# Performance work log

Hardware: AMD Instinct MI355X
Metric: run time of the kernel (lower is better)

Reference implementation:

```python
import jax, jax.numpy as jnp
import numpy as np

jax.config.update("jax_enable_x64", True)

# Module hyperparameters (from init_kwargs)
NUM_EMB = 1_000_000
EMB_DIM = 128
COMPRESSION = 1.0 / 64.0
WEIGHT_SIZE = int(NUM_EMB * EMB_DIM * COMPRESSION)  # 2_000_000 (1D compressed table)

# Hash constants matching the CUDA kernel's multiplicative hash:
# hashed_idx = (index * P1 + dim * P2) mod weight_size
P1 = np.uint64(9824516537)
P2 = np.uint64(57857966300227)

BATCH = 16384
BAG_LEN = 50


def _hashed_idx(indices):
    # indices: [N] int -> hashed positions [N, EMB_DIM] into the 1D weight table
    flat = indices.reshape(-1).astype(jnp.uint64)
    dims = jnp.arange(EMB_DIM, dtype=jnp.uint64)
    h = (flat[:, None] * P1 + dims[None, :] * P2) % jnp.uint64(WEIGHT_SIZE)
    return h.astype(jnp.int64)


def setup_inputs() -> dict:
    key = jax.random.key(0)
    k1, k2 = jax.random.split(key)
    indices = jax.random.randint(k1, (BATCH, BAG_LEN), 0, NUM_EMB, dtype=jnp.int64)
    # reset_parameters(): init.normal_(weight)
    weight = jax.random.normal(k2, (WEIGHT_SIZE,), dtype=jnp.float32)
    return {"weight": weight, "indices": indices}


def reference(weight, indices):
    # 2D indices path: each row is one bag of fixed length; mode='sum'.
    B, L = indices.shape
    hidx = _hashed_idx(indices)                      # [B*L, D]
    emb = weight[hidx].reshape(B, L, EMB_DIM)        # gather from compressed table
    return emb.sum(axis=1)                           # [B, D] per-bag sum
```

## Files before the change

kernel.cpp:

```cpp
#include <hip/hip_runtime.h>
#include <stdint.h>


#define WS       2000000
#define EMB_DIM  128
#define BAG_LEN  50
#define BATCH    16384

#define NBLK     256
#define NTHR     1024
#define BAGS_PB  64
#define NPAIR    32
#define SPT      4
#define EXTP     208
#define THALF    32768
#define NREGD    62
#define SBIG     300227u
#define SENT     0x10000000u

#define OFF_T1   65536
#define OFF_EXT  131072
#define SMEM_SZ  157696

#define GLOAD_LDS16(gp, lp)                                            \
    __builtin_amdgcn_global_load_lds(                                  \
        (const __attribute__((address_space(1))) uint32_t*)(gp),       \
        (__attribute__((address_space(3))) uint32_t*)(lp), 16, 0, 0)

__global__ __launch_bounds__(1024) void conv_bf16(
    const float* __restrict__ w, uint16_t* __restrict__ o)
{
    const int i = (blockIdx.x * 1024 + threadIdx.x) * 4;
    if (i >= WS) return;
    const float4 f = *(const float4*)(w + i);
    uint32_t u0 = __float_as_uint(f.x), u1 = __float_as_uint(f.y);
    uint32_t u2 = __float_as_uint(f.z), u3 = __float_as_uint(f.w);
    ushort4 r;
    r.x = (uint16_t)((u0 + 0x7FFFu + ((u0 >> 16) & 1u)) >> 16);
    r.y = (uint16_t)((u1 + 0x7FFFu + ((u1 >> 16) & 1u)) >> 16);
    r.z = (uint16_t)((u2 + 0x7FFFu + ((u2 >> 16) & 1u)) >> 16);
    r.w = (uint16_t)((u3 + 0x7FFFu + ((u3 >> 16) & 1u)) >> 16);
    *(ushort4*)(o + i) = r;
}

__global__ __launch_bounds__(NTHR, 4) void heb_bf16(
    const uint16_t* __restrict__ wbf,
    const int*      __restrict__ indices,
    float*          __restrict__ out)
{
    __shared__ __align__(16) uint8_t smem[SMEM_SZ];

    const int tid     = threadIdx.x;
    const int d       = tid & 127;
    const int g       = tid >> 7;
    const int bagBase = blockIdx.x * BAGS_PB;

    uint16_t* tile0 = (uint16_t*)&smem[0];
    uint32_t* ext   = (uint32_t*)&smem[OFF_EXT];
    uint32_t* araw  = (uint32_t*)&smem[OFF_T1];
    uint32_t* S     = (uint32_t*)&smem[OFF_T1 + 13312];

    for (int s = tid; s < (THALF >> 3); s += NTHR)
        GLOAD_LDS16(wbf + (s << 3), tile0 + (s << 3));

    for (int p = tid; p < NPAIR * EXTP; p += NTHR) ext[p] = SENT;
    for (int p = tid; p < BAGS_PB * BAG_LEN; p += NTHR) {
        uint32_t b = (uint32_t)p / 50u;
        uint32_t i = (uint32_t)p - b * 50u;
        uint64_t idx = (uint64_t)(uint32_t)indices[bagBase * BAG_LEN + p];
        araw[b * 52 + i] = (uint32_t)((idx * 9824516537ull) % (uint64_t)WS);
    }
    __syncthreads();

    for (int p = tid; p < BAGS_PB * BAG_LEN; p += NTHR) {
        uint32_t b = (uint32_t)p / 50u;
        uint32_t i = (uint32_t)p - b * 50u;
        uint32_t v = araw[b * 52 + i];
        int rank = 0;
        for (int q = 0; q < BAG_LEN; ++q) {
            uint32_t w = araw[b * 52 + q];
            rank += (w < v || (w == v && q < (int)i)) ? 1 : 0;
        }
        S[b * 52 + rank] = v;
    }
    __syncthreads();

    for (int p = tid; p < BAGS_PB * BAG_LEN; p += NTHR) {
        uint32_t bag = (uint32_t)p / 50u;
        uint32_t i   = (uint32_t)p - bag * 50u;
        uint32_t pr  = bag >> 1, b = bag & 1u;
        uint32_t v = S[bag * 52 + i];
        const uint32_t* T = &S[(bag ^ 1u) * 52];
        uint32_t key = b ? v + 1u : v;
        int lo = 0, hi = 50;
        while (lo < hi) {
            int mid = (lo + hi) >> 1;
            bool lt = T[mid] < key;
            lo = lt ? mid + 1 : lo;
            hi = lt ? hi : mid;
        }
        uint32_t* eo = ext + pr * EXTP;
        int rk = (int)i + lo;
        eo[rk]       = (v << 1) | b;
        eo[rk + 100] = ((v + (uint32_t)WS) << 1) | b;
    }
    __syncthreads();

    const uint32_t c  = ((uint32_t)d * SBIG) % (uint32_t)WS;
    const uint32_t C2 = (uint32_t)(((int)c - WS) * 2);
    const uint32_t limit2 = ((uint32_t)WS - c) << 1;

    const char* kp4[SPT];
    uint32_t    K4[SPT];
    float       s0r[SPT], s1r[SPT];
#pragma unroll
    for (int qi = 0; qi < SPT; ++qi) {
        const uint32_t* eo = ext + ((g << 2) + qi) * EXTP;
        int lo = 0, hi = 100;
        while (lo < hi) {
            int mid = (lo + hi) >> 1;
            bool lt = eo[mid] < limit2;
            lo = lt ? mid + 1 : lo;
            hi = lt ? hi : mid;
        }
        kp4[qi] = (const char*)(eo + lo);
        K4[qi]  = eo[lo];
        s0r[qi] = 0.0f; s1r[qi] = 0.0f;
    }
    __syncthreads();

    for (int r = 0; r < NREGD; ++r) {
        if (r + 1 < NREGD) {
            const int lo2  = (r + 1) * THALF;
            const int len2 = (THALF < WS - lo2) ? THALF : (WS - lo2);
            uint16_t* dst = (uint16_t*)&smem[((r + 1) & 1) ? OFF_T1 : 0];
            for (int s = tid; s < (len2 >> 3); s += NTHR)
                GLOAD_LDS16(wbf + lo2 + (s << 3), dst + (s << 3));
        }

        const int rlo = r * THALF;
        const int len = (THALF < WS - rlo) ? THALF : (WS - rlo);
        const uint32_t TB  = (r & 1) ? (uint32_t)OFF_T1 : 0u;
        const uint32_t CLr = C2 + TB - ((uint32_t)rlo << 1);
        const uint32_t LIM = ((uint32_t)len << 1) + TB;

#pragma unroll
        for (int qi = 0; qi < SPT; ++qi) {
            const char* kp = kp4[qi];
            uint32_t K_ = K4[qi];
            float s0 = s0r[qi], s1 = s1r[qi];
            uint32_t u = K_ + CLr;
            while (u < LIM) {
                const uint32_t raw =
                    *(const uint16_t*)(smem + (u & ~1u));
                kp += 4;
                const uint32_t Kn = *(const uint32_t*)kp;
                const float v = __uint_as_float(raw << 16);
                const bool odd = (u & 1u) != 0u;
                s0 += odd ? 0.0f : v;
                s1 += odd ? v : 0.0f;
                K_ = Kn;
                u  = Kn + CLr;
            }
            kp4[qi] = kp; K4[qi] = K_;
            s0r[qi] = s0; s1r[qi] = s1;
        }
        __syncthreads();
    }

#pragma unroll
    for (int qi = 0; qi < SPT; ++qi) {
        const int bag = (g << 3) + (qi << 1);
        out[(size_t)(bagBase + bag) * EMB_DIM + d]     = s0r[qi];
        out[(size_t)(bagBase + bag + 1) * EMB_DIM + d] = s1r[qi];
    }
}

#define RSIZE_FB 32768
#define NREG_FB  62
#define EXT_N    104
#define SENT4    0x10000000u

__global__ __launch_bounds__(NTHR, 4) void heb_single(
    const float* __restrict__ weight,
    const int*   __restrict__ indices,
    float*       __restrict__ out)
{
    __shared__ __align__(16) float tile[RSIZE_FB];
    __shared__ uint32_t ext4[BAGS_PB][EXT_N];
    const int tid = threadIdx.x, d = tid & 127, bag_lo = tid >> 7;
    const int bagBase = blockIdx.x * BAGS_PB;
    uint32_t* araw = (uint32_t*)&tile[0];
    for (int p = tid; p < BAGS_PB * BAG_LEN; p += NTHR) {
        uint32_t g = (uint32_t)p / 50u, i = (uint32_t)p - g * 50u;
        uint64_t idx = (uint64_t)(uint32_t)indices[bagBase * BAG_LEN + p];
        araw[g * 52 + i] = (uint32_t)((idx * 9824516537ull) % (uint64_t)WS);
    }
    __syncthreads();
    for (int p = tid; p < BAGS_PB * BAG_LEN; p += NTHR) {
        uint32_t g = (uint32_t)p / 50u, i = (uint32_t)p - g * 50u;
        uint32_t v = araw[g * 52 + i];
        int rank = 0;
        for (int q = 0; q < BAG_LEN; ++q) {
            uint32_t w = araw[g * 52 + q];
            rank += (w < v || (w == v && q < (int)i)) ? 1 : 0;
        }
        ext4[g][rank] = v << 2;
        ext4[g][rank + 50] = (v + (uint32_t)WS) << 2;
    }
    for (int p = tid; p < BAGS_PB * 4; p += NTHR)
        ext4[p >> 2][100 + (p & 3)] = SENT4;
    __syncthreads();
    const uint32_t c = ((uint32_t)d * SBIG) % (uint32_t)WS;
    const uint32_t C4 = (uint32_t)(((int)c - WS) * 4);
    const uint32_t wmc4 = ((uint32_t)WS - c) << 2;
    uint32_t t4[8], h4[8]; float sm[8];
#pragma unroll
    for (int k = 0; k < 8; ++k) {
        const uint32_t* eg = &ext4[(bag_lo << 3) + k][0];
        int nlow = 0;
        for (int q = 0; q < BAG_LEN; ++q) nlow += (eg[q] < wmc4) ? 1 : 0;
        t4[k] = (uint32_t)nlow << 2; h4[k] = eg[nlow] + C4; sm[k] = 0.0f;
    }
    for (int r = 0; r < NREG_FB; ++r) {
        const int lo = r * RSIZE_FB;
        const int len = (RSIZE_FB < WS - lo) ? RSIZE_FB : (WS - lo);
        __syncthreads();
        for (int s = tid; s < (len >> 2); s += NTHR)
            GLOAD_LDS16(weight + lo + (s << 2), &tile[s << 2]);
        __syncthreads();
        const uint32_t lo4 = ((uint32_t)lo) << 2;
        const uint32_t hi4 = (r == NREG_FB - 1) ? (uint32_t)(4 * WS)
                                                : lo4 + ((uint32_t)RSIZE_FB << 2);
        const char* tb = (const char*)&tile[0];
#pragma unroll
        for (int k = 0; k < 8; ++k) {
            const char* eg = (const char*)&ext4[(bag_lo << 3) + k][0];
            uint32_t t_ = t4[k], h_ = h4[k]; float s_ = sm[k];
            while (h_ < hi4) {
                s_ += *(const float*)(tb + (h_ - lo4));
                t_ += 4u;
                h_ = *(const uint32_t*)(eg + t_) + C4;
            }
            t4[k] = t_; h4[k] = h_; sm[k] = s_;
        }
    }
#pragma unroll
    for (int k = 0; k < 8; ++k)
        out[(size_t)(bagBase + (bag_lo << 3) + k) * EMB_DIM + d] = sm[k];
}

extern "C" void kernel_launch(void* const* d_in, const int* in_sizes, int n_in,
                              void* d_out, int out_size, void* d_ws, size_t ws_size,
                              hipStream_t stream)
{
    const float* weight  = (const float*)d_in[0];
    const int*   indices = (const int*)d_in[1];
    float*       out     = (float*)d_out;

    if (ws_size >= (size_t)WS * sizeof(uint16_t)) {
        uint16_t* wbf = (uint16_t*)d_ws;
        conv_bf16<<<(WS / 4 + 1023) / 1024, 1024, 0, stream>>>(weight, wbf);
        heb_bf16<<<NBLK, NTHR, 0, stream>>>(wbf, indices, out);
    } else {
        heb_single<<<NBLK, NTHR, 0, stream>>>(weight, indices, out);
    }
}
```

Before: 230.0 us.

## Split block work: sweep 48 bags through LDS, gather 16 bags directly from global

Each block now sends only 48 of its 64 bags through the region-sweeping LDS scheme, which walks the whole bf16 table in 62 regions. The other two thread groups gather the remaining 16 bags straight from the global bf16 table, one bag element per region iteration, which overlaps random global loads with the LDS sweep. The intent is to spread the sweep's work over fewer bags and to use the otherwise idle memory bandwidth for direct gathers. In exchange it adds load imbalance between the two kinds of thread groups and uncoalesced global accesses, and the extension-list pointer is now an index.

```diff
diff --git a/kernel.cpp b/kernel.cpp
--- a/kernel.cpp
+++ b/kernel.cpp
@@ -10,7 +10,9 @@
 #define NBLK     256
 #define NTHR     1024
 #define BAGS_PB  64
-#define NPAIR    32
+#define SWBAGS   48
+#define GBAGS    16
+#define NPAIR    24
 #define SPT      4
 #define EXTP     208
 #define THALF    32768
@@ -20,7 +22,8 @@
 
 #define OFF_T1   65536
 #define OFF_EXT  131072
-#define SMEM_SZ  157696
+#define OFF_AG   151040
+#define SMEM_SZ  154240
 
 #define GLOAD_LDS16(gp, lp)                                            \
     __builtin_amdgcn_global_load_lds(                                  \
@@ -57,8 +60,9 @@
 
     uint16_t* tile0 = (uint16_t*)&smem[0];
     uint32_t* ext   = (uint32_t*)&smem[OFF_EXT];
+    uint32_t* ag    = (uint32_t*)&smem[OFF_AG];
     uint32_t* araw  = (uint32_t*)&smem[OFF_T1];
-    uint32_t* S     = (uint32_t*)&smem[OFF_T1 + 13312];
+    uint32_t* S     = (uint32_t*)&smem[OFF_T1 + 9984];
 
     for (int s = tid; s < (THALF >> 3); s += NTHR)
         GLOAD_LDS16(wbf + (s << 3), tile0 + (s << 3));
@@ -68,11 +72,13 @@
         uint32_t b = (uint32_t)p / 50u;
         uint32_t i = (uint32_t)p - b * 50u;
         uint64_t idx = (uint64_t)(uint32_t)indices[bagBase * BAG_LEN + p];
-        araw[b * 52 + i] = (uint32_t)((idx * 9824516537ull) % (uint64_t)WS);
-    }
-    __syncthreads();
-
-    for (int p = tid; p < BAGS_PB * BAG_LEN; p += NTHR) {
+        uint32_t a = (uint32_t)((idx * 9824516537ull) % (uint64_t)WS);
+        if (b < SWBAGS) araw[b * 52 + i] = a;
+        else            ag[(b - SWBAGS) * 50 + i] = a;
+    }
+    __syncthreads();
+
+    for (int p = tid; p < SWBAGS * BAG_LEN; p += NTHR) {
         uint32_t b = (uint32_t)p / 50u;
         uint32_t i = (uint32_t)p - b * 50u;
         uint32_t v = araw[b * 52 + i];
@@ -85,7 +91,7 @@
     }
     __syncthreads();
 
-    for (int p = tid; p < BAGS_PB * BAG_LEN; p += NTHR) {
+    for (int p = tid; p < SWBAGS * BAG_LEN; p += NTHR) {
         uint32_t bag = (uint32_t)p / 50u;
         uint32_t i   = (uint32_t)p - bag * 50u;
         uint32_t pr  = bag >> 1, b = bag & 1u;
@@ -110,22 +116,36 @@
     const uint32_t C2 = (uint32_t)(((int)c - WS) * 2);
     const uint32_t limit2 = ((uint32_t)WS - c) << 1;
 
-    const char* kp4[SPT];
-    uint32_t    K4[SPT];
-    float       s0r[SPT], s1r[SPT];
-#pragma unroll
-    for (int qi = 0; qi < SPT; ++qi) {
-        const uint32_t* eo = ext + ((g << 2) + qi) * EXTP;
-        int lo = 0, hi = 100;
-        while (lo < hi) {
-            int mid = (lo + hi) >> 1;
-            bool lt = eo[mid] < limit2;
-            lo = lt ? mid + 1 : lo;
-            hi = lt ? hi : mid;
-        }
-        kp4[qi] = (const char*)(eo + lo);
-        K4[qi]  = eo[lo];
-        s0r[qi] = 0.0f; s1r[qi] = 0.0f;
+    uint32_t kq4[SPT] = {0, 0, 0, 0}, K4[SPT] = {0, 0, 0, 0};
+    float    s0r[SPT] = {0, 0, 0, 0}, s1r[SPT] = {0, 0, 0, 0};
+    uint32_t gck[8];
+    float    gacc[8];
+    int      bagG = 0, agB = 0, d0 = 0;
+
+    if (g < 6) {
+#pragma unroll
+        for (int qi = 0; qi < SPT; ++qi) {
+            const uint32_t rbase = (uint32_t)((g << 2) + qi) * EXTP;
+            int lo = 0, hi = 100;
+            while (lo < hi) {
+                int mid = (lo + hi) >> 1;
+                bool lt = ext[rbase + (uint32_t)mid] < limit2;
+                lo = lt ? mid + 1 : lo;
+                hi = lt ? hi : mid;
+            }
+            kq4[qi] = rbase + (uint32_t)lo;
+            K4[qi]  = ext[rbase + (uint32_t)lo];
+        }
+    } else {
+        const int L = tid & 127;
+        bagG = (g << 3) + (L >> 4);
+        d0   = L & 15;
+        agB  = (bagG - SWBAGS) * 50;
+#pragma unroll
+        for (int k = 0; k < 8; ++k) {
+            gck[k]  = ((uint32_t)(d0 + 16 * k) * SBIG) % (uint32_t)WS;
+            gacc[k] = 0.0f;
+        }
     }
     __syncthreads();
 
@@ -138,41 +158,57 @@
                 GLOAD_LDS16(wbf + lo2 + (s << 3), dst + (s << 3));
         }
 
-        const int rlo = r * THALF;
-        const int len = (THALF < WS - rlo) ? THALF : (WS - rlo);
-        const uint32_t TB  = (r & 1) ? (uint32_t)OFF_T1 : 0u;
-        const uint32_t CLr = C2 + TB - ((uint32_t)rlo << 1);
-        const uint32_t LIM = ((uint32_t)len << 1) + TB;
-
+        if (g < 6) {
+            const int rlo = r * THALF;
+            const int len = (THALF < WS - rlo) ? THALF : (WS - rlo);
+            const uint32_t TB  = (r & 1) ? (uint32_t)OFF_T1 : 0u;
+            const uint32_t CLr = C2 + TB - ((uint32_t)rlo << 1);
+            const uint32_t LIM = ((uint32_t)len << 1) + TB;
+
+#pragma unroll
+            for (int qi = 0; qi < SPT; ++qi) {
+                uint32_t kq = kq4[qi], K = K4[qi];
+                float s0 = s0r[qi], s1 = s1r[qi];
+                uint32_t u = K + CLr;
+                while (u < LIM) {
+                    const uint32_t raw =
+                        *(const uint16_t*)(smem + (u & ~1u));
+                    K = ext[kq + 1u];
+                    ++kq;
+                    const float v = __uint_as_float(raw << 16);
+                    const bool odd = (u & 1u) != 0u;
+                    s0 += odd ? 0.0f : v;
+                    s1 += odd ? v : 0.0f;
+                    u = K + CLr;
+                }
+                kq4[qi] = kq; K4[qi] = K;
+                s0r[qi] = s0; s1r[qi] = s1;
+            }
+        } else if (r < BAG_LEN) {
+            const uint32_t a = ag[agB + r];
+#pragma unroll
+            for (int k = 0; k < 8; ++k) {
+                uint32_t u = a + gck[k];
+                u = (u >= (uint32_t)WS) ? u - (uint32_t)WS : u;
+                const uint32_t raw = (uint32_t)wbf[u];
+                gacc[k] += __uint_as_float(raw << 16);
+            }
+        }
+        __syncthreads();
+    }
+
+    if (g < 6) {
 #pragma unroll
         for (int qi = 0; qi < SPT; ++qi) {
-            const char* kp = kp4[qi];
-            uint32_t K_ = K4[qi];
-            float s0 = s0r[qi], s1 = s1r[qi];
-            uint32_t u = K_ + CLr;
-            while (u < LIM) {
-                const uint32_t raw =
-                    *(const uint16_t*)(smem + (u & ~1u));
-                kp += 4;
-                const uint32_t Kn = *(const uint32_t*)kp;
-                const float v = __uint_as_float(raw << 16);
-                const bool odd = (u & 1u) != 0u;
-                s0 += odd ? 0.0f : v;
-                s1 += odd ? v : 0.0f;
-                K_ = Kn;
-                u  = Kn + CLr;
-            }
-            kp4[qi] = kp; K4[qi] = K_;
-            s0r[qi] = s0; s1r[qi] = s1;
-        }
-        __syncthreads();
-    }
-
-#pragma unroll
-    for (int qi = 0; qi < SPT; ++qi) {
-        const int bag = (g << 3) + (qi << 1);
-        out[(size_t)(bagBase + bag) * EMB_DIM + d]     = s0r[qi];
-        out[(size_t)(bagBase + bag + 1) * EMB_DIM + d] = s1r[qi];
+            const int bag = (g << 3) + (qi << 1);
+            out[(size_t)(bagBase + bag) * EMB_DIM + d]     = s0r[qi];
+            out[(size_t)(bagBase + bag + 1) * EMB_DIM + d] = s1r[qi];
+        }
+    } else {
+#pragma unroll
+        for (int k = 0; k < 8; ++k)
+            out[(size_t)(bagBase + bagG) * EMB_DIM + (d0 + 16 * k)] =
+                gacc[k];
     }
 }
 
```

After: 236.6 us. 2.8% more time.

## Split bags between LDS-streaming blocks and direct-gather blocks, shrink tile for occupancy

Applied to the files above, without the earlier changes.

The bag work is split in two. 48 of each 64-bag group stay on the LDS-streaming path, and the other 16 bags go to 256 extra blocks that gather bf16 weights straight from global memory. The streaming path drops double buffering and uses one smaller single tile, so LDS use falls enough to allow 8 blocks per CU. In exchange it adds two barriers per region and more regions. The aim is to overlap the random-gather blocks with the streaming blocks and raise occupancy, at the cost of serialising the tile load with compute.

```diff
diff --git a/kernel.cpp b/kernel.cpp
--- a/kernel.cpp
+++ b/kernel.cpp
@@ -7,20 +7,21 @@
 #define BAG_LEN  50
 #define BATCH    16384
 
-#define NBLK     256
+#define NBLK     512
+#define NBLK_SW  256
 #define NTHR     1024
 #define BAGS_PB  64
-#define NPAIR    32
-#define SPT      4
-#define EXTP     208
-#define THALF    32768
-#define NREGD    62
+#define SWBAGS   48
+#define NPAIR    24
+#define SPT      3
+#define EXTP     204
+#define TILEE    28672
+#define NREGS    70
 #define SBIG     300227u
 #define SENT     0x10000000u
 
-#define OFF_T1   65536
-#define OFF_EXT  131072
-#define SMEM_SZ  157696
+#define OFF_EXT  57344
+#define SMEM_SZ  76928
 
 #define GLOAD_LDS16(gp, lp)                                            \
     __builtin_amdgcn_global_load_lds(                                  \
@@ -43,36 +44,69 @@
     *(ushort4*)(o + i) = r;
 }
 
-__global__ __launch_bounds__(NTHR, 4) void heb_bf16(
+__global__ __launch_bounds__(NTHR, 8) void heb_bf16(
     const uint16_t* __restrict__ wbf,
     const int*      __restrict__ indices,
     float*          __restrict__ out)
 {
     __shared__ __align__(16) uint8_t smem[SMEM_SZ];
-
-    const int tid     = threadIdx.x;
+    const int tid = threadIdx.x;
+
+    if (blockIdx.x >= NBLK_SW) {
+        const int gi   = blockIdx.x - NBLK_SW;
+        const int bagL = tid >> 6;
+        const int d0   = tid & 63;
+        uint32_t* ag = (uint32_t*)smem;
+
+        for (int p = tid; p < 16 * BAG_LEN; p += NTHR) {
+            int b = p / 50, i = p - b * 50;
+            uint64_t idx = (uint64_t)(uint32_t)
+                indices[(gi * BAGS_PB + SWBAGS + b) * BAG_LEN + i];
+            ag[p] = (uint32_t)((idx * 9824516537ull) % (uint64_t)WS);
+        }
+        __syncthreads();
+
+        const uint32_t c0 = ((uint32_t)d0 * SBIG) % (uint32_t)WS;
+        const uint32_t c1 = ((uint32_t)(d0 + 64) * SBIG) % (uint32_t)WS;
+        const uint32_t* agb = ag + bagL * BAG_LEN;
+        float a0 = 0.0f, a1 = 0.0f;
+#pragma unroll 10
+        for (int i = 0; i < BAG_LEN; ++i) {
+            const uint32_t a = agb[i];
+            uint32_t u0 = a + c0; u0 = (u0 >= (uint32_t)WS) ? u0 - WS : u0;
+            uint32_t u1 = a + c1; u1 = (u1 >= (uint32_t)WS) ? u1 - WS : u1;
+            const uint32_t r0 = (uint32_t)wbf[u0];
+            const uint32_t r1 = (uint32_t)wbf[u1];
+            a0 += __uint_as_float(r0 << 16);
+            a1 += __uint_as_float(r1 << 16);
+        }
+        const size_t ob =
+            (size_t)(gi * BAGS_PB + SWBAGS + bagL) * EMB_DIM;
+        out[ob + d0]      = a0;
+        out[ob + d0 + 64] = a1;
+        return;
+    }
+
     const int d       = tid & 127;
     const int g       = tid >> 7;
     const int bagBase = blockIdx.x * BAGS_PB;
 
     uint16_t* tile0 = (uint16_t*)&smem[0];
     uint32_t* ext   = (uint32_t*)&smem[OFF_EXT];
-    uint32_t* araw  = (uint32_t*)&smem[OFF_T1];
-    uint32_t* S     = (uint32_t*)&smem[OFF_T1 + 13312];
-
-    for (int s = tid; s < (THALF >> 3); s += NTHR)
-        GLOAD_LDS16(wbf + (s << 3), tile0 + (s << 3));
+    uint32_t* araw  = (uint32_t*)&smem[0];
+    uint32_t* S     = (uint32_t*)&smem[9984];
 
     for (int p = tid; p < NPAIR * EXTP; p += NTHR) ext[p] = SENT;
-    for (int p = tid; p < BAGS_PB * BAG_LEN; p += NTHR) {
+    for (int p = tid; p < SWBAGS * BAG_LEN; p += NTHR) {
         uint32_t b = (uint32_t)p / 50u;
         uint32_t i = (uint32_t)p - b * 50u;
-        uint64_t idx = (uint64_t)(uint32_t)indices[bagBase * BAG_LEN + p];
+        uint64_t idx = (uint64_t)(uint32_t)
+            indices[bagBase * BAG_LEN + p];
         araw[b * 52 + i] = (uint32_t)((idx * 9824516537ull) % (uint64_t)WS);
     }
     __syncthreads();
 
-    for (int p = tid; p < BAGS_PB * BAG_LEN; p += NTHR) {
+    for (int p = tid; p < SWBAGS * BAG_LEN; p += NTHR) {
         uint32_t b = (uint32_t)p / 50u;
         uint32_t i = (uint32_t)p - b * 50u;
         uint32_t v = araw[b * 52 + i];
@@ -85,7 +119,7 @@
     }
     __syncthreads();
 
-    for (int p = tid; p < BAGS_PB * BAG_LEN; p += NTHR) {
+    for (int p = tid; p < SWBAGS * BAG_LEN; p += NTHR) {
         uint32_t bag = (uint32_t)p / 50u;
         uint32_t i   = (uint32_t)p - bag * 50u;
         uint32_t pr  = bag >> 1, b = bag & 1u;
@@ -110,67 +144,59 @@
     const uint32_t C2 = (uint32_t)(((int)c - WS) * 2);
     const uint32_t limit2 = ((uint32_t)WS - c) << 1;
 
-    const char* kp4[SPT];
-    uint32_t    K4[SPT];
-    float       s0r[SPT], s1r[SPT];
+    uint32_t kq4[SPT], K4[SPT];
+    float    s0r[SPT], s1r[SPT];
 #pragma unroll
     for (int qi = 0; qi < SPT; ++qi) {
-        const uint32_t* eo = ext + ((g << 2) + qi) * EXTP;
+        const uint32_t rbase = (uint32_t)(g * SPT + qi) * EXTP;
         int lo = 0, hi = 100;
         while (lo < hi) {
             int mid = (lo + hi) >> 1;
-            bool lt = eo[mid] < limit2;
+            bool lt = ext[rbase + (uint32_t)mid] < limit2;
             lo = lt ? mid + 1 : lo;
             hi = lt ? hi : mid;
         }
-        kp4[qi] = (const char*)(eo + lo);
-        K4[qi]  = eo[lo];
+        kq4[qi] = rbase + (uint32_t)lo;
+        K4[qi]  = ext[rbase + (uint32_t)lo];
         s0r[qi] = 0.0f; s1r[qi] = 0.0f;
     }
-    __syncthreads();
-
-    for (int r = 0; r < NREGD; ++r) {
-        if (r + 1 < NREGD) {
-            const int lo2  = (r + 1) * THALF;
-            const int len2 = (THALF < WS - lo2) ? THALF : (WS - lo2);
-            uint16_t* dst = (uint16_t*)&smem[((r + 1) & 1) ? OFF_T1 : 0];
-            for (int s = tid; s < (len2 >> 3); s += NTHR)
-                GLOAD_LDS16(wbf + lo2 + (s << 3), dst + (s << 3));
-        }
-
-        const int rlo = r * THALF;
-        const int len = (THALF < WS - rlo) ? THALF : (WS - rlo);
-        const uint32_t TB  = (r & 1) ? (uint32_t)OFF_T1 : 0u;
-        const uint32_t CLr = C2 + TB - ((uint32_t)rlo << 1);
-        const uint32_t LIM = ((uint32_t)len << 1) + TB;
+
+    for (int r = 0; r < NREGS; ++r) {
+        const int rlo = r * TILEE;
+        const int len = (TILEE < WS - rlo) ? TILEE : (WS - rlo);
+
+        __syncthreads();
+        for (int s = tid; s < (len >> 3); s += NTHR)
+            GLOAD_LDS16(wbf + rlo + (s << 3), tile0 + (s << 3));
+        __syncthreads();
+
+        const uint32_t CLr = C2 - ((uint32_t)rlo << 1);
+        const uint32_t LIM = (uint32_t)len << 1;
 
 #pragma unroll
         for (int qi = 0; qi < SPT; ++qi) {
-            const char* kp = kp4[qi];
-            uint32_t K_ = K4[qi];
+            uint32_t kq = kq4[qi], K = K4[qi];
             float s0 = s0r[qi], s1 = s1r[qi];
-            uint32_t u = K_ + CLr;
+            uint32_t u = K + CLr;
             while (u < LIM) {
                 const uint32_t raw =
                     *(const uint16_t*)(smem + (u & ~1u));
-                kp += 4;
-                const uint32_t Kn = *(const uint32_t*)kp;
+                K = ext[kq + 1u];
+                ++kq;
                 const float v = __uint_as_float(raw << 16);
                 const bool odd = (u & 1u) != 0u;
                 s0 += odd ? 0.0f : v;
                 s1 += odd ? v : 0.0f;
-                K_ = Kn;
-                u  = Kn + CLr;
+                u = K + CLr;
             }
-            kp4[qi] = kp; K4[qi] = K_;
+            kq4[qi] = kq; K4[qi] = K;
             s0r[qi] = s0; s1r[qi] = s1;
         }
-        __syncthreads();
     }
 
 #pragma unroll
     for (int qi = 0; qi < SPT; ++qi) {
-        const int bag = (g << 3) + (qi << 1);
+        const int bag = g * 6 + (qi << 1);
         out[(size_t)(bagBase + bag) * EMB_DIM + d]     = s0r[qi];
         out[(size_t)(bagBase + bag + 1) * EMB_DIM + d] = s1r[qi];
     }
```

Measured after the change: 254.3 us. 1.11x slower.
